# Optimization experiments

Hardware: AMD Instinct MI355X
Metric: run time of the kernel (lower is better)

Reference implementation:

```python
import jax, jax.numpy as jnp
import numpy as np

N, D, H, O, E, TOP_K = 8192, 1024, 2048, 1024, 8, 2


def setup_inputs() -> dict:
    key = jax.random.key(0)
    ks = jax.random.split(key, 8)
    s = lambda fan: 1.0 / np.sqrt(fan)
    return {
        "x": jax.random.normal(ks[0], (N, D), jnp.float32),
        "W1": jax.random.normal(ks[1], (E, D, H), jnp.float32) * s(D),
        "b1": jnp.zeros((E, H), jnp.float32),
        "W2": jax.random.normal(ks[2], (E, H, H), jnp.float32) * s(H),
        "b2": jnp.zeros((E, H), jnp.float32),
        "W3": jax.random.normal(ks[3], (E, H, O), jnp.float32) * s(H),
        "b3": jnp.zeros((E, O), jnp.float32),
        "Wg1": jax.random.normal(ks[4], (D, 64), jnp.float32) * s(D),
        "bg1": jnp.zeros((64,), jnp.float32),
        "Wg2": jax.random.normal(ks[5], (64, E), jnp.float32) * s(64),
        "bg2": jnp.zeros((E,), jnp.float32),
        "top_k": TOP_K,
    }


def reference(x, W1, b1, W2, b2, W3, b3, Wg1, bg1, Wg2, bg2, top_k):
    # Gating network: Linear -> relu -> Linear -> softmax over experts
    gates = jax.nn.softmax(jax.nn.relu(x @ Wg1 + bg1) @ Wg2 + bg2, axis=1)  # [N, E]
    # Top-k membership mask per token (combine weight is the ORIGINAL gate value,
    # matching the torch code which ignores the renormalized top_k_gates)
    _, top_idx = jax.lax.top_k(gates, top_k)                       # [N, k]
    num_experts = gates.shape[1]
    in_topk = (top_idx[:, :, None] == jnp.arange(num_experts)[None, None, :]).any(axis=1)  # [N, E]
    w = jnp.where(in_topk, gates, 0.0)                             # [N, E]
    # Expert MLPs (dropout is identity at inference). Dense over experts;
    # combine zeros out non-selected experts, matching the masked dispatch math.
    h = jax.nn.relu(jnp.einsum("nd,edh->enh", x, W1) + b1[:, None, :])   # [E, N, H]
    h = jax.nn.relu(jnp.einsum("enh,ehk->enk", h, W2) + b2[:, None, :])  # [E, N, H]
    y = jnp.einsum("enh,eho->eno", h, W3) + b3[:, None, :]               # [E, N, O]
    return jnp.einsum("eno,ne->no", y, w)                                # [N, O]
```

## Files before the change

### kernel.cpp

```cpp
#include <hip/hip_runtime.h>

typedef _Float16 fp16_t;
typedef __attribute__((ext_vector_type(8))) _Float16 f16x8;
typedef __attribute__((ext_vector_type(4))) _Float16 f16x4;
typedef __attribute__((ext_vector_type(4))) float f32x4;

#define N_TOK 8192
#define DIM   1024
#define HID   2048
#define OUTD  1024
#define NE    8
#define NPAIR 16384
#define MAXSLOT 72
#define HBLK 64

__device__ __forceinline__ void load_lds16(const void* g, void* l) {
    __builtin_amdgcn_global_load_lds(
        (__attribute__((address_space(1))) void*)g,
        (__attribute__((address_space(3))) void*)l, 16, 0, 0);
}

__global__ __launch_bounds__(256) void gating_kernel(
    const float* __restrict__ x,  const float* __restrict__ Wg1,
    const float* __restrict__ bg1, const float* __restrict__ Wg2,
    const float* __restrict__ bg2,
    int* __restrict__ top_i, float* __restrict__ top_w)
{
    __shared__ float xs[8][DIM];
    const int tid = threadIdx.x, lane = tid & 63, wv = tid >> 6;

    const float4* x4 = (const float4*)(x + (size_t)blockIdx.x * 8 * DIM);
    float4* xs4 = (float4*)&xs[0][0];
    #pragma unroll
    for (int i = 0; i < 8; ++i) xs4[tid + 256 * i] = x4[tid + 256 * i];
    __syncthreads();

    const int trow = wv * 2;
    const float b = bg1[lane];
    float h00 = b,   h01 = 0.f;
    float h10 = b,   h11 = 0.f;
    for (int d0 = 0; d0 < DIM; d0 += 8) {
        float w[8];
        #pragma unroll
        for (int i = 0; i < 8; ++i) w[i] = Wg1[(d0 + i) * 64 + lane];
        float4 a00 = *(const float4*)&xs[trow][d0];
        float4 a01 = *(const float4*)&xs[trow][d0 + 4];
        float4 a10 = *(const float4*)&xs[trow + 1][d0];
        float4 a11 = *(const float4*)&xs[trow + 1][d0 + 4];
        h00 = fmaf(a00.x, w[0], fmaf(a00.y, w[1], fmaf(a00.z, w[2], fmaf(a00.w, w[3], h00))));
        h01 = fmaf(a01.x, w[4], fmaf(a01.y, w[5], fmaf(a01.z, w[6], fmaf(a01.w, w[7], h01))));
        h10 = fmaf(a10.x, w[0], fmaf(a10.y, w[1], fmaf(a10.z, w[2], fmaf(a10.w, w[3], h10))));
        h11 = fmaf(a11.x, w[4], fmaf(a11.y, w[5], fmaf(a11.z, w[6], fmaf(a11.w, w[7], h11))));
    }
    float hg[2] = { h00 + h01, h10 + h11 };

    #pragma unroll
    for (int t = 0; t < 2; ++t) {
        float h = fmaxf(hg[t], 0.f);
        float p[NE];
        #pragma unroll
        for (int e = 0; e < NE; ++e) p[e] = h * Wg2[lane * NE + e];
        #pragma unroll
        for (int s = 32; s > 0; s >>= 1) {
            #pragma unroll
            for (int e = 0; e < NE; ++e) p[e] += __shfl_xor(p[e], s, 64);
        }
        if (lane == 0) {
            int n = blockIdx.x * 8 + trow + t;
            float g[NE];
            float m = -1e30f;
            #pragma unroll
            for (int e = 0; e < NE; ++e) { g[e] = p[e] + bg2[e]; m = fmaxf(m, g[e]); }
            float s = 0.f;
            #pragma unroll
            for (int e = 0; e < NE; ++e) { g[e] = expf(g[e] - m); s += g[e]; }
            float inv = 1.f / s;
            #pragma unroll
            for (int e = 0; e < NE; ++e) g[e] *= inv;
            int b0 = 0;
            #pragma unroll
            for (int e = 1; e < NE; ++e) if (g[e] > g[b0]) b0 = e;
            int b1 = (b0 == 0) ? 1 : 0;
            #pragma unroll
            for (int e = 0; e < NE; ++e) if (e != b0 && g[e] > g[b1]) b1 = e;
            top_i[n] = b0;          top_i[N_TOK + n] = b1;
            top_w[n] = g[b0];       top_w[N_TOK + n] = g[b1];
        }
    }
}

__global__ __launch_bounds__(256) void hist_kernel(
    const int* __restrict__ top_i, int* __restrict__ blockhist)
{
    __shared__ int wh[4][NE];
    const int tid = threadIdx.x, lane = tid & 63, wv = tid >> 6;
    const int e = top_i[blockIdx.x * 256 + tid];
    #pragma unroll
    for (int e0 = 0; e0 < NE; ++e0) {
        unsigned long long m = __ballot(e == e0);
        if (lane == 0) wh[wv][e0] = __popcll(m);
    }
    __syncthreads();
    if (tid < NE)
        blockhist[blockIdx.x * NE + tid] =
            wh[0][tid] + wh[1][tid] + wh[2][tid] + wh[3][tid];
}

__global__ __launch_bounds__(512) void scan_kernel(
    const int* __restrict__ blockhist, int* __restrict__ offs,
    int* __restrict__ pairbase,
    int* __restrict__ tile_e, int* __restrict__ tile_mt)
{
    __shared__ int h[HBLK * NE], pb[HBLK * NE], off_s[NE + 1];
    const int tid = threadIdx.x;
    h[tid] = blockhist[tid];
    __syncthreads();
    if (tid == 0) {
        int c[NE] = {};
        for (int b = 0; b < HBLK; ++b)
            #pragma unroll
            for (int e = 0; e < NE; ++e) { pb[b * NE + e] = c[e]; c[e] += h[b * NE + e]; }
        int acc = 0;
        #pragma unroll
        for (int e = 0; e < NE; ++e) { off_s[e] = acc; acc += c[e]; }
        off_s[NE] = acc;
        for (int e = 0; e <= NE; ++e) offs[e] = off_s[e];
        int s = 0;
        for (int e = 0; e < NE; ++e) {
            int nt = (c[e] + 255) >> 8;
            for (int mt = 0; mt < nt; ++mt) { tile_e[s] = e; tile_mt[s] = mt; ++s; }
        }
        for (; s < MAXSLOT; ++s) tile_e[s] = -1;
    }
    __syncthreads();
    pairbase[tid] = pb[tid] + off_s[tid & (NE - 1)];
}

__global__ __launch_bounds__(256) void scatter_kernel(
    const int* __restrict__ top_i, const int* __restrict__ pairbase,
    int* __restrict__ pair_token, int* __restrict__ slot)
{
    __shared__ int wh[4][NE];
    const int tid = threadIdx.x, lane = tid & 63, wv = tid >> 6;
    const int p = blockIdx.x * 256 + tid;
    const int e = top_i[p];
    int myrank = 0;
    #pragma unroll
    for (int e0 = 0; e0 < NE; ++e0) {
        unsigned long long m = __ballot(e == e0);
        if (lane == 0) wh[wv][e0] = __popcll(m);
        if (e == e0) myrank = __popcll(m & ((1ull << lane) - 1ull));
    }
    __syncthreads();
    int wprefix = 0;
    for (int w = 0; w < wv; ++w) wprefix += wh[w][e];
    const int pout = pairbase[blockIdx.x * NE + e] + wprefix + myrank;
    pair_token[pout] = p & (N_TOK - 1);
    slot[p] = pout;
}

__global__ __launch_bounds__(256) void xcvt_kernel(
    const float* __restrict__ x, fp16_t* __restrict__ xb)
{
    size_t i = ((size_t)blockIdx.x * 256 + threadIdx.x) * 4;
    float4 v = *(const float4*)(x + i);
    f16x4 o = { (fp16_t)v.x, (fp16_t)v.y, (fp16_t)v.z, (fp16_t)v.w };
    *(f16x4*)(xb + i) = o;
}

__global__ __launch_bounds__(256) void transpose_cvt(
    const float* __restrict__ src, fp16_t* __restrict__ dst, int R, int C)
{
    int bb = blockIdx.z;
    src += (size_t)bb * R * C;
    dst += (size_t)bb * R * C;
    __shared__ float sm[32][33];
    int tx = threadIdx.x & 31, ty = threadIdx.x >> 5;
    int r0 = blockIdx.y * 32, c0 = blockIdx.x * 32;
    #pragma unroll
    for (int i = 0; i < 4; ++i)
        sm[ty + 8 * i][tx] = src[(size_t)(r0 + ty + 8 * i) * C + c0 + tx];
    __syncthreads();
    #pragma unroll
    for (int i = 0; i < 4; ++i)
        dst[(size_t)(c0 + ty + 8 * i) * R + r0 + tx] = (fp16_t)sm[tx][ty + 8 * i];
}

template <int K, int NOUT, bool GATHER, bool RELU, bool OUT_FP16>
__global__ __launch_bounds__(512) void gemm_expert(
    const fp16_t* __restrict__ A, const fp16_t* __restrict__ Wt,
    const float* __restrict__ bias, void* __restrict__ Cout,
    const int* __restrict__ offs, const int* __restrict__ pair_token,
    const int* __restrict__ tile_e, const int* __restrict__ tile_mt)
{
    const int e = tile_e[blockIdx.y];
    if (e < 0) return;
    const int mt  = tile_mt[blockIdx.y];
    const int off = offs[e];
    const int cnt = offs[e + 1] - off;
    const int rows_here = min(256, cnt - mt * 256);
    const int mb = off + mt * 256;
    const int n0 = blockIdx.x * 256;

    extern __shared__ __align__(16) char smem[];

    const int tid = threadIdx.x, lane = tid & 63, wv = tid >> 6;
    const int wm = wv >> 2, wn = wv & 3;
    const int l15 = lane & 15, quad = lane >> 4, sb = l15 & 7;

    const int rowsel = tid >> 3;
    const int coff = ((tid & 7) ^ (rowsel & 7)) * 8;

    const fp16_t* We = Wt + (size_t)e * NOUT * K;

    const fp16_t* aptr[2][2];
    #pragma unroll
    for (int h = 0; h < 2; ++h)
        #pragma unroll
        for (int s = 0; s < 2; ++s) {
            int tr = rowsel + s * 128 + h * 64;
            int rc = (tr < rows_here) ? tr : (rows_here - 1);
            long rowidx = GATHER ? (long)pair_token[mb + rc] : (long)(mb + rc);
            aptr[h][s] = A + rowidx * (long)K + coff;
        }
    const int nbase = (rowsel & 31) + (tid >> 8) * 64;
    const fp16_t* bptr = We + (size_t)(n0 + nbase) * K + coff;

    char* const ldsw = smem + wv * 1024;

#define STAGE_A(h, kt) do {                                                  \
        int _b = ((kt) & 1) * 32768 + (h) * 16384;                           \
        load_lds16(aptr[h][0] + (kt) * 64, ldsw + _b);                       \
        load_lds16(aptr[h][1] + (kt) * 64, ldsw + _b + 8192); } while (0)

#define STAGE_B(h, kt) do {                                                  \
        int _b = 65536 + ((kt) & 1) * 32768 + (h) * 16384;                   \
        load_lds16(bptr + (size_t)((h) * 32) * K + (kt) * 64, ldsw + _b);    \
        load_lds16(bptr + (size_t)((h) * 32 + 128) * K + (kt) * 64,          \
                   ldsw + _b + 8192); } while (0)

    const int slot0 = (quad ^ sb) * 16;
    const int slot1 = ((quad + 4) ^ sb) * 16;
    const int arow = (wm * 64 + l15) * 128;
    const int brow = (wn * 32 + l15) * 128;

    f16x8 a[4][2], b0[2][2], b1[2][2];
    f32x4 acc[8][4] = {};

#define READ_A(buf, h) do {                                                  \
        _Pragma("unroll")                                                    \
        for (int ii = 0; ii < 4; ++ii) {                                     \
            int _b = (buf) * 32768 + (h) * 16384 + arow + ii * 2048;         \
            a[ii][0] = *(const f16x8*)(smem + _b + slot0);                   \
            a[ii][1] = *(const f16x8*)(smem + _b + slot1);                   \
        } } while (0)

#define READ_B(buf, h, br) do {                                              \
        _Pragma("unroll")                                                    \
        for (int jj = 0; jj < 2; ++jj) {                                     \
            int _b = 65536 + (buf) * 32768 + (h) * 16384 + brow + jj * 2048; \
            br[jj][0] = *(const f16x8*)(smem + _b + slot0);                  \
            br[jj][1] = *(const f16x8*)(smem + _b + slot1);                  \
        } } while (0)

#define MFMA_Q(imb, jnb, br) do {                                            \
        _Pragma("unroll")                                                    \
        for (int ks = 0; ks < 2; ++ks)                                       \
        _Pragma("unroll")                                                    \
        for (int ii = 0; ii < 4; ++ii)                                       \
        _Pragma("unroll")                                                    \
        for (int jj = 0; jj < 2; ++jj)                                       \
            acc[(imb) + ii][(jnb) + jj] =                                    \
                __builtin_amdgcn_mfma_f32_16x16x32_f16(                      \
                    a[ii][ks], br[jj][ks], acc[(imb) + ii][(jnb) + jj],      \
                    0, 0, 0); } while (0)

#define BAR() do { asm volatile("" ::: "memory");                            \
                   __builtin_amdgcn_s_barrier();                             \
                   asm volatile("" ::: "memory"); } while (0)
#define VM0()   asm volatile("s_waitcnt vmcnt(0)" ::: "memory")

    STAGE_A(0, 0); STAGE_A(1, 0); STAGE_B(0, 0); STAGE_B(1, 0);
    VM0();
    BAR();

    const int ntile = K / 64;
    for (int t = 0; t < ntile; ++t) {
        const int buf = t & 1;
        if (t + 1 < ntile) {
            STAGE_A(0, t + 1); STAGE_A(1, t + 1);
            STAGE_B(0, t + 1); STAGE_B(1, t + 1);
        }
        READ_A(buf, 0); READ_B(buf, 0, b0);
        MFMA_Q(0, 0, b0);
        READ_B(buf, 1, b1);
        MFMA_Q(0, 2, b1);
        READ_A(buf, 1);
        MFMA_Q(4, 2, b1);
        MFMA_Q(4, 0, b0);
        VM0();
        BAR();
    }

#undef STAGE_A
#undef STAGE_B
#undef READ_A
#undef READ_B
#undef MFMA_Q
#undef BAR
#undef VM0

    const float* be = bias + (size_t)e * NOUT + n0;
    #pragma unroll
    for (int j = 0; j < 4; ++j) {
        int col = wn * 64 + j * 16 + l15;
        float bv = be[col];
        #pragma unroll
        for (int i2 = 0; i2 < 8; ++i2) {
            int mrow0 = wm * 128 + i2 * 16 + quad * 4;
            #pragma unroll
            for (int r = 0; r < 4; ++r) {
                int m = mrow0 + r;
                if (m < rows_here) {
                    float v = acc[i2][j][r] + bv;
                    if (RELU) v = fmaxf(v, 0.f);
                    size_t o = (size_t)(mb + m) * NOUT + n0 + col;
                    if (OUT_FP16) ((fp16_t*)Cout)[o] = (fp16_t)v;
                    else          ((float*)Cout)[o]  = v;
                }
            }
        }
    }
}

__global__ __launch_bounds__(256) void combine_kernel(
    const float* __restrict__ y, const int* __restrict__ slot,
    const float* __restrict__ top_w, float* __restrict__ out)
{
    int idx = blockIdx.x * 256 + threadIdx.x;
    int n  = idx >> 8;
    int o4 = idx & 255;
    int s0 = slot[n], s1 = slot[N_TOK + n];
    float w0 = top_w[n], w1 = top_w[N_TOK + n];
    float4 y0 = *(const float4*)(y + (size_t)s0 * OUTD + o4 * 4);
    float4 y1 = *(const float4*)(y + (size_t)s1 * OUTD + o4 * 4);
    float4 r;
    r.x = w0 * y0.x + w1 * y1.x;
    r.y = w0 * y0.y + w1 * y1.y;
    r.z = w0 * y0.z + w1 * y1.z;
    r.w = w0 * y0.w + w1 * y1.w;
    *(float4*)(out + (size_t)n * OUTD + o4 * 4) = r;
}

extern "C" void kernel_launch(void* const* d_in, const int* in_sizes, int n_in,
                              void* d_out, int out_size, void* d_ws, size_t ws_size,
                              hipStream_t stream)
{
    (void)in_sizes; (void)n_in; (void)out_size; (void)ws_size;
    const float* x   = (const float*)d_in[0];
    const float* W1  = (const float*)d_in[1];
    const float* b1  = (const float*)d_in[2];
    const float* W2  = (const float*)d_in[3];
    const float* b2  = (const float*)d_in[4];
    const float* W3  = (const float*)d_in[5];
    const float* b3  = (const float*)d_in[6];
    const float* Wg1 = (const float*)d_in[7];
    const float* bg1 = (const float*)d_in[8];
    const float* Wg2 = (const float*)d_in[9];
    const float* bg2 = (const float*)d_in[10];

    char* ws = (char*)d_ws;
    fp16_t* xb = (fp16_t*)ws;
    fp16_t* h1 = (fp16_t*)(ws + 16777216);
    fp16_t* h2 = (fp16_t*)(ws + 83886080);
    fp16_t* Wt = (fp16_t*)(ws + 150994944);
    char* rt   = ws + 218103808;
    int*   offs       = (int*)rt;
    int*   tile_e     = offs + 9;
    int*   tile_mt    = tile_e + MAXSLOT;
    int*   top_i      = tile_mt + MAXSLOT;
    float* top_w      = (float*)(top_i + 2 * N_TOK);
    int*   slot       = (int*)(top_w + 2 * N_TOK);
    int*   pair_token = slot + 2 * N_TOK;
    int*   blockhist  = pair_token + NPAIR;
    int*   pairbase   = blockhist + HBLK * NE;

    gating_kernel<<<1024, 256, 0, stream>>>(x, Wg1, bg1, Wg2, bg2, top_i, top_w);
    hist_kernel<<<HBLK, 256, 0, stream>>>(top_i, blockhist);
    scan_kernel<<<1, HBLK * NE, 0, stream>>>(blockhist, offs, pairbase, tile_e, tile_mt);
    scatter_kernel<<<HBLK, 256, 0, stream>>>(top_i, pairbase, pair_token, slot);
    xcvt_kernel<<<8192, 256, 0, stream>>>(x, xb);

    transpose_cvt<<<dim3(HID / 32, DIM / 32, NE), 256, 0, stream>>>(W1, Wt, DIM, HID);
    gemm_expert<DIM, HID, true, true, true>
        <<<dim3(HID / 256, MAXSLOT), 512, 131072, stream>>>(
            xb, Wt, b1, (void*)h1, offs, pair_token, tile_e, tile_mt);

    transpose_cvt<<<dim3(HID / 32, HID / 32, NE), 256, 0, stream>>>(W2, Wt, HID, HID);
    gemm_expert<HID, HID, false, true, true>
        <<<dim3(HID / 256, MAXSLOT), 512, 131072, stream>>>(
            h1, Wt, b2, (void*)h2, offs, pair_token, tile_e, tile_mt);

    transpose_cvt<<<dim3(OUTD / 32, HID / 32, NE), 256, 0, stream>>>(W3, Wt, HID, OUTD);
    gemm_expert<HID, OUTD, false, false, false>
        <<<dim3(OUTD / 256, MAXSLOT), 512, 131072, stream>>>(
            h2, Wt, b3, (void*)h1, offs, pair_token, tile_e, tile_mt);

    combine_kernel<<<8192, 256, 0, stream>>>((const float*)h1, slot, top_w, (float*)d_out);
}
```

Baseline: 863.3 us.

## Shrink expert GEMM tile to 256x128 with K=32 steps for higher occupancy

Reworks the grouped expert GEMM from a 256x256 output tile with 64-wide K steps and 128KB of LDS to a 256x128 tile with 32-wide K steps and 48KB of LDS. The launch bound now requests more resident waves, with each wave computing a 64x64 sub-tile. The goal is more concurrent blocks per CU, to hide latency and to balance work across the many per-expert tiles. In exchange, each loaded byte is reused less, so global and LDS traffic per FLOP goes up. There are also twice as many barriers per unit of K.

```diff
diff --git a/kernel.cpp b/kernel.cpp
--- a/kernel.cpp
+++ b/kernel.cpp
@@ -187,7 +187,7 @@
 }
 
 template <int K, int NOUT, bool GATHER, bool RELU, bool OUT_FP16>
-__global__ __launch_bounds__(512) void gemm_expert(
+__global__ __launch_bounds__(512, 4) void gemm_expert(
     const fp16_t* __restrict__ A, const fp16_t* __restrict__ Wt,
     const float* __restrict__ bias, void* __restrict__ Cout,
     const int* __restrict__ offs, const int* __restrict__ pair_token,
@@ -200,129 +200,101 @@
     const int cnt = offs[e + 1] - off;
     const int rows_here = min(256, cnt - mt * 256);
     const int mb = off + mt * 256;
-    const int n0 = blockIdx.x * 256;
+    const int n0 = blockIdx.x * 128;
 
     extern __shared__ __align__(16) char smem[];
 
     const int tid = threadIdx.x, lane = tid & 63, wv = tid >> 6;
-    const int wm = wv >> 2, wn = wv & 3;
-    const int l15 = lane & 15, quad = lane >> 4, sb = l15 & 7;
-
-    const int rowsel = tid >> 3;
-    const int coff = ((tid & 7) ^ (rowsel & 7)) * 8;
+    const int wm = wv >> 1, wn = wv & 1;
+    const int l15 = lane & 15, quad = lane >> 4;
+
+    const int coff = ((lane & 3) ^ ((lane >> 3) & 3)) * 8;
 
     const fp16_t* We = Wt + (size_t)e * NOUT * K;
 
-    const fp16_t* aptr[2][2];
-    #pragma unroll
-    for (int h = 0; h < 2; ++h)
-        #pragma unroll
-        for (int s = 0; s < 2; ++s) {
-            int tr = rowsel + s * 128 + h * 64;
-            int rc = (tr < rows_here) ? tr : (rows_here - 1);
-            long rowidx = GATHER ? (long)pair_token[mb + rc] : (long)(mb + rc);
-            aptr[h][s] = A + rowidx * (long)K + coff;
-        }
-    const int nbase = (rowsel & 31) + (tid >> 8) * 64;
-    const fp16_t* bptr = We + (size_t)(n0 + nbase) * K + coff;
-
-    char* const ldsw = smem + wv * 1024;
-
-#define STAGE_A(h, kt) do {                                                  \
-        int _b = ((kt) & 1) * 32768 + (h) * 16384;                           \
-        load_lds16(aptr[h][0] + (kt) * 64, ldsw + _b);                       \
-        load_lds16(aptr[h][1] + (kt) * 64, ldsw + _b + 8192); } while (0)
-
-#define STAGE_B(h, kt) do {                                                  \
-        int _b = 65536 + ((kt) & 1) * 32768 + (h) * 16384;                   \
-        load_lds16(bptr + (size_t)((h) * 32) * K + (kt) * 64, ldsw + _b);    \
-        load_lds16(bptr + (size_t)((h) * 32 + 128) * K + (kt) * 64,          \
-                   ldsw + _b + 8192); } while (0)
-
-    const int slot0 = (quad ^ sb) * 16;
-    const int slot1 = ((quad + 4) ^ sb) * 16;
-    const int arow = (wm * 64 + l15) * 128;
-    const int brow = (wn * 32 + l15) * 128;
-
-    f16x8 a[4][2], b0[2][2], b1[2][2];
-    f32x4 acc[8][4] = {};
-
-#define READ_A(buf, h) do {                                                  \
+    const fp16_t* aptr[2];
+    #pragma unroll
+    for (int s = 0; s < 2; ++s) {
+        int tr = wv * 16 + (lane >> 2) + s * 128;
+        int rc = (tr < rows_here) ? tr : (rows_here - 1);
+        long rowidx = GATHER ? (long)pair_token[mb + rc] : (long)(mb + rc);
+        aptr[s] = A + rowidx * (long)K + coff;
+    }
+    const int nrow = n0 + wv * 16 + (lane >> 2);
+    const fp16_t* bptr = We + (size_t)nrow * K + coff;
+
+    char* const asw = smem + wv * 1024;
+    char* const bsw = smem + 32768 + wv * 1024;
+
+#define STAGE(kt) do {                                                       \
+        int _ab = ((kt) & 1) * 16384;                                        \
+        int _bb = ((kt) & 1) * 8192;                                         \
+        load_lds16(aptr[0] + (kt) * 32, asw + _ab);                          \
+        load_lds16(aptr[1] + (kt) * 32, asw + _ab + 8192);                   \
+        load_lds16(bptr    + (kt) * 32, bsw + _bb); } while (0)
+
+    const int slotc = quad ^ ((l15 >> 1) & 3);
+    const int arow = (wm * 64 + l15) * 64 + slotc * 16;
+    const int brow = (wn * 64 + l15) * 64 + slotc * 16;
+
+    f16x8 a[4], b[4];
+    f32x4 acc[4][4] = {};
+
+#define READ(buf) do {                                                       \
         _Pragma("unroll")                                                    \
-        for (int ii = 0; ii < 4; ++ii) {                                     \
-            int _b = (buf) * 32768 + (h) * 16384 + arow + ii * 2048;         \
-            a[ii][0] = *(const f16x8*)(smem + _b + slot0);                   \
-            a[ii][1] = *(const f16x8*)(smem + _b + slot1);                   \
-        } } while (0)
-
-#define READ_B(buf, h, br) do {                                              \
+        for (int ii = 0; ii < 4; ++ii)                                       \
+            a[ii] = *(const f16x8*)(smem + (buf) * 16384 + arow + ii * 1024);\
         _Pragma("unroll")                                                    \
-        for (int jj = 0; jj < 2; ++jj) {                                     \
-            int _b = 65536 + (buf) * 32768 + (h) * 16384 + brow + jj * 2048; \
-            br[jj][0] = *(const f16x8*)(smem + _b + slot0);                  \
-            br[jj][1] = *(const f16x8*)(smem + _b + slot1);                  \
-        } } while (0)
-
-#define MFMA_Q(imb, jnb, br) do {                                            \
-        _Pragma("unroll")                                                    \
-        for (int ks = 0; ks < 2; ++ks)                                       \
+        for (int jj = 0; jj < 4; ++jj)                                       \
+            b[jj] = *(const f16x8*)(smem + 32768 + (buf) * 8192 + brow       \
+                                    + jj * 1024); } while (0)
+
+#define MFMA_ALL() do {                                                      \
         _Pragma("unroll")                                                    \
         for (int ii = 0; ii < 4; ++ii)                                       \
         _Pragma("unroll")                                                    \
-        for (int jj = 0; jj < 2; ++jj)                                       \
-            acc[(imb) + ii][(jnb) + jj] =                                    \
-                __builtin_amdgcn_mfma_f32_16x16x32_f16(                      \
-                    a[ii][ks], br[jj][ks], acc[(imb) + ii][(jnb) + jj],      \
-                    0, 0, 0); } while (0)
+        for (int jj = 0; jj < 4; ++jj)                                       \
+            acc[ii][jj] = __builtin_amdgcn_mfma_f32_16x16x32_f16(            \
+                a[ii], b[jj], acc[ii][jj], 0, 0, 0); } while (0)
 
 #define BAR() do { asm volatile("" ::: "memory");                            \
                    __builtin_amdgcn_s_barrier();                             \
                    asm volatile("" ::: "memory"); } while (0)
 #define VM0()   asm volatile("s_waitcnt vmcnt(0)" ::: "memory")
 
-    STAGE_A(0, 0); STAGE_A(1, 0); STAGE_B(0, 0); STAGE_B(1, 0);
+    STAGE(0);
     VM0();
     BAR();
 
-    const int ntile = K / 64;
+    const int ntile = K / 32;
     for (int t = 0; t < ntile; ++t) {
         const int buf = t & 1;
-        if (t + 1 < ntile) {
-            STAGE_A(0, t + 1); STAGE_A(1, t + 1);
-            STAGE_B(0, t + 1); STAGE_B(1, t + 1);
-        }
-        READ_A(buf, 0); READ_B(buf, 0, b0);
-        MFMA_Q(0, 0, b0);
-        READ_B(buf, 1, b1);
-        MFMA_Q(0, 2, b1);
-        READ_A(buf, 1);
-        MFMA_Q(4, 2, b1);
-        MFMA_Q(4, 0, b0);
+        if (t + 1 < ntile) STAGE(t + 1);
+        READ(buf);
+        MFMA_ALL();
         VM0();
         BAR();
     }
 
-#undef STAGE_A
-#undef STAGE_B
-#undef READ_A
-#undef READ_B
-#undef MFMA_Q
+#undef STAGE
+#undef READ
+#undef MFMA_ALL
 #undef BAR
 #undef VM0
 
     const float* be = bias + (size_t)e * NOUT + n0;
     #pragma unroll
-    for (int j = 0; j < 4; ++j) {
-        int col = wn * 64 + j * 16 + l15;
+    for (int jj = 0; jj < 4; ++jj) {
+        int col = wn * 64 + jj * 16 + l15;
         float bv = be[col];
         #pragma unroll
-        for (int i2 = 0; i2 < 8; ++i2) {
-            int mrow0 = wm * 128 + i2 * 16 + quad * 4;
+        for (int ii = 0; ii < 4; ++ii) {
+            int mrow0 = wm * 64 + ii * 16 + quad * 4;
             #pragma unroll
             for (int r = 0; r < 4; ++r) {
                 int m = mrow0 + r;
                 if (m < rows_here) {
-                    float v = acc[i2][j][r] + bv;
+                    float v = acc[ii][jj][r] + bv;
                     if (RELU) v = fmaxf(v, 0.f);
                     size_t o = (size_t)(mb + m) * NOUT + n0 + col;
                     if (OUT_FP16) ((fp16_t*)Cout)[o] = (fp16_t)v;
@@ -393,17 +365,17 @@
 
     transpose_cvt<<<dim3(HID / 32, DIM / 32, NE), 256, 0, stream>>>(W1, Wt, DIM, HID);
     gemm_expert<DIM, HID, true, true, true>
-        <<<dim3(HID / 256, MAXSLOT), 512, 131072, stream>>>(
+        <<<dim3(HID / 128, MAXSLOT), 512, 49152, stream>>>(
             xb, Wt, b1, (void*)h1, offs, pair_token, tile_e, tile_mt);
 
     transpose_cvt<<<dim3(HID / 32, HID / 32, NE), 256, 0, stream>>>(W2, Wt, HID, HID);
     gemm_expert<HID, HID, false, true, true>
-        <<<dim3(HID / 256, MAXSLOT), 512, 131072, stream>>>(
+        <<<dim3(HID / 128, MAXSLOT), 512, 49152, stream>>>(
             h1, Wt, b2, (void*)h2, offs, pair_token, tile_e, tile_mt);
 
     transpose_cvt<<<dim3(OUTD / 32, HID / 32, NE), 256, 0, stream>>>(W3, Wt, HID, OUTD);
     gemm_expert<HID, OUTD, false, false, false>
-        <<<dim3(OUTD / 256, MAXSLOT), 512, 131072, stream>>>(
+        <<<dim3(OUTD / 128, MAXSLOT), 512, 49152, stream>>>(
             h2, Wt, b3, (void*)h1, offs, pair_token, tile_e, tile_mt);
 
     combine_kernel<<<8192, 256, 0, stream>>>((const float*)h1, slot, top_w, (float*)d_out);
```

After: 876.2 us. Within noise of the previous version (+1.5%).

## Restructure GEMM main loop into an 8-phase pipelined schedule with finer-grained prefetch

Applied to the files above, without the earlier changes.

Replaces the simple double-buffered K loop with a loop unrolled by two tiles and split into eight phases. Each phase interleaves LDS reads, staging of quarter-tiles of the next tile, barriers and MFMA clusters. Waits use vmcnt(6) so some global loads stay in flight, and s_setprio raises wave priority around the MFMA blocks. This aims to overlap global-to-LDS transfers with compute, at the cost of many more barriers and a tighter buffer-reuse ordering that could race if the stage and read slots are sequenced incorrectly.

```diff
diff --git a/kernel.cpp b/kernel.cpp
--- a/kernel.cpp
+++ b/kernel.cpp
@@ -278,27 +278,58 @@
 #define BAR() do { asm volatile("" ::: "memory");                            \
                    __builtin_amdgcn_s_barrier();                             \
                    asm volatile("" ::: "memory"); } while (0)
+#define LGKM0() asm volatile("s_waitcnt lgkmcnt(0)" ::: "memory")
+#define VM6()   asm volatile("s_waitcnt vmcnt(6)" ::: "memory")
 #define VM0()   asm volatile("s_waitcnt vmcnt(0)" ::: "memory")
 
-    STAGE_A(0, 0); STAGE_A(1, 0); STAGE_B(0, 0); STAGE_B(1, 0);
-    VM0();
+    STAGE_A(0, 0); STAGE_B(0, 0); STAGE_B(1, 0); STAGE_A(1, 0);
+    STAGE_A(0, 1); STAGE_B(0, 1); STAGE_B(1, 1);
+    VM6();
     BAR();
 
-    const int ntile = K / 64;
-    for (int t = 0; t < ntile; ++t) {
-        const int buf = t & 1;
-        if (t + 1 < ntile) {
-            STAGE_A(0, t + 1); STAGE_A(1, t + 1);
-            STAGE_B(0, t + 1); STAGE_B(1, t + 1);
-        }
-        READ_A(buf, 0); READ_B(buf, 0, b0);
-        MFMA_Q(0, 0, b0);
-        READ_B(buf, 1, b1);
-        MFMA_Q(0, 2, b1);
-        READ_A(buf, 1);
-        MFMA_Q(4, 2, b1);
-        MFMA_Q(4, 0, b0);
-        VM0();
+    const int niter = K / 128;
+    for (int i = 0; i < niter; ++i) {
+        const int kt0 = 2 * i, kt1 = kt0 + 1;
+        const bool pf = (i + 1 < niter);
+        READ_A(0, 0); READ_B(0, 0, b0);
+        STAGE_A(1, kt1);
+        BAR(); LGKM0();
+        __builtin_amdgcn_s_setprio(1); MFMA_Q(0, 0, b0); __builtin_amdgcn_s_setprio(0);
+        BAR();
+        READ_B(0, 1, b1);
+        if (pf) STAGE_A(0, kt0 + 2);
+        BAR(); LGKM0();
+        __builtin_amdgcn_s_setprio(1); MFMA_Q(0, 2, b1); __builtin_amdgcn_s_setprio(0);
+        BAR();
+        READ_A(0, 1);
+        if (pf) STAGE_B(0, kt0 + 2);
+        BAR(); LGKM0();
+        __builtin_amdgcn_s_setprio(1); MFMA_Q(4, 2, b1); __builtin_amdgcn_s_setprio(0);
+        BAR();
+        if (pf) STAGE_B(1, kt0 + 2);
+        BAR();
+        __builtin_amdgcn_s_setprio(1); MFMA_Q(4, 0, b0); __builtin_amdgcn_s_setprio(0);
+        if (pf) VM6(); else VM0();
+        BAR();
+        READ_A(1, 0); READ_B(1, 0, b0);
+        if (pf) STAGE_A(1, kt0 + 2);
+        BAR(); LGKM0();
+        __builtin_amdgcn_s_setprio(1); MFMA_Q(0, 0, b0); __builtin_amdgcn_s_setprio(0);
+        BAR();
+        READ_B(1, 1, b1);
+        if (pf) STAGE_A(0, kt0 + 3);
+        BAR(); LGKM0();
+        __builtin_amdgcn_s_setprio(1); MFMA_Q(0, 2, b1); __builtin_amdgcn_s_setprio(0);
+        BAR();
+        READ_A(1, 1);
+        if (pf) STAGE_B(0, kt0 + 3);
+        BAR(); LGKM0();
+        __builtin_amdgcn_s_setprio(1); MFMA_Q(4, 2, b1); __builtin_amdgcn_s_setprio(0);
+        BAR();
+        if (pf) STAGE_B(1, kt0 + 3);
+        BAR();
+        __builtin_amdgcn_s_setprio(1); MFMA_Q(4, 0, b0); __builtin_amdgcn_s_setprio(0);
+        if (pf) VM6(); else VM0();
         BAR();
     }
 
@@ -308,6 +339,8 @@
 #undef READ_B
 #undef MFMA_Q
 #undef BAR
+#undef LGKM0
+#undef VM6
 #undef VM0
 
     const float* be = bias + (size_t)e * NOUT + n0;
```

New measurement: 858.8 us. Within noise of the previous version (-0.5%).
